# Performance work log

Measured on AMD Instinct MI355X. Metric: run time of the kernel, lower is better.

## Reference

```python
import jax, jax.numpy as jnp
import numpy as np

BS, T, D_IN = 128, 32, 128
DH = 128          # controller hidden size == memory word width M
N_SLOTS = 512     # memory rows
EPS = 1e-8


def _split_read(o):
    # o: [bs, M+6] -> k, beta, g, s(3), gamma
    k = o[:, :DH]
    beta = jax.nn.softplus(o[:, DH])
    g = jax.nn.sigmoid(o[:, DH + 1])
    s = jax.nn.softmax(o[:, DH + 2:DH + 5], axis=-1)
    gamma = 1.0 + jax.nn.softplus(o[:, DH + 5])
    return k, beta, g, s, gamma


def _attention(k, beta, g, s, gamma, mem, w_prev):
    # content addressing: cosine similarity sharpened by beta
    dot = jnp.einsum('bnm,bm->bn', mem, k)
    denom = jnp.linalg.norm(mem, axis=-1) * jnp.linalg.norm(k, axis=-1, keepdims=True) + EPS
    w_c = jax.nn.softmax(beta[:, None] * dot / denom, axis=-1)
    # gate interpolation with previous weights
    w_g = g[:, None] * w_c + (1.0 - g[:, None]) * w_prev
    # circular shift convolution over offsets {-1, 0, +1}
    w_t = (s[:, 0:1] * jnp.roll(w_g, -1, axis=-1)
           + s[:, 1:2] * w_g
           + s[:, 2:3] * jnp.roll(w_g, 1, axis=-1))
    # sharpening
    w = w_t ** gamma[:, None]
    return w / (jnp.sum(w, axis=-1, keepdims=True) + EPS)


def setup_inputs() -> dict:
    key = jax.random.key(0)
    ks = jax.random.split(key, 8)
    sc = lambda fan_in: 1.0 / np.sqrt(fan_in)
    return {
        'x':    jax.random.normal(ks[0], (BS, T, D_IN), jnp.float32),
        'Wxh':  jax.random.normal(ks[1], (D_IN, DH), jnp.float32) * sc(D_IN),
        'Whh':  jax.random.normal(ks[2], (DH, DH), jnp.float32) * sc(DH),
        'Wrh':  jax.random.normal(ks[3], (DH, DH), jnp.float32) * sc(DH),
        'bh':   jnp.zeros((DH,), jnp.float32),
        'Wout': jax.random.normal(ks[4], (DH + DH, D_IN), jnp.float32) * sc(2 * DH),
        'bout': jnp.zeros((D_IN,), jnp.float32),
        'Wr':   jax.random.normal(ks[5], (DH, DH + 6), jnp.float32) * sc(DH),
        'br':   jnp.zeros((DH + 6,), jnp.float32),
        'Ww':   jax.random.normal(ks[6], (DH, 3 * DH + 6), jnp.float32) * sc(DH),
        'bw':   jnp.zeros((3 * DH + 6,), jnp.float32),
    }


def reference(x, Wxh, Whh, Wrh, bh, Wout, bout, Wr, br, Ww, bw):
    bs = x.shape[0]
    h0 = jnp.zeros((bs, DH), x.dtype)
    r0 = jnp.zeros((bs, DH), x.dtype)
    w0 = jnp.full((bs, N_SLOTS), 1.0 / N_SLOTS, x.dtype)
    mem0 = jnp.full((bs, N_SLOTS, DH), 1e-6, x.dtype)

    def step(carry, x_t):
        h, r, w_prev, mem = carry
        # controller state
        h = jnp.tanh(x_t @ Wxh + h @ Whh + r @ Wrh + bh)
        # head parameter projections
        o_r = h @ Wr + br
        o_w = h @ Ww + bw
        k_r, b_r, g_r, s_r, y_r = _split_read(o_r)
        k_w, b_w_, g_w, s_w, y_w = _split_read(o_w[:, :DH + 6])
        e = jax.nn.sigmoid(o_w[:, DH + 6:2 * DH + 6])   # erase [bs, M]
        a = jnp.tanh(o_w[:, 2 * DH + 6:3 * DH + 6])     # add   [bs, M]
        # addressing (w_previous updated sequentially, read then write)
        w_r = _attention(k_r, b_r, g_r, s_r, y_r, mem, w_prev)
        w_w = _attention(k_w, b_w_, g_w, s_w, y_w, mem, w_r)
        # read
        r = jnp.einsum('bn,bnm->bm', w_r, mem)
        # erase / add write
        mem = mem * (1.0 - w_w[:, :, None] * e[:, None, :]) + w_w[:, :, None] * a[:, None, :]
        # output
        y = jnp.concatenate([h, r], axis=-1) @ Wout + bout
        return (h, r, w_w, mem), y

    _, ys = jax.lax.scan(step, (h0, r0, w0, mem0), jnp.swapaxes(x, 0, 1))
    return jnp.swapaxes(ys, 0, 1)  # [bs, ft, d_output]
```

## Files before the change

### kernel.cpp

```cpp
#include <hip/hip_runtime.h>
#include <hip/hip_bf16.h>
#include <math.h>

#define NT 1024
#define BSZ 128
#define TSTEPS 32
#define DIN 128
#define DHH 128
#define NSLOT 512
#define EPSF 1e-8f

static constexpr int F_FLOATS = 7160;
static constexpr size_t LDS_BYTES = 131072 + F_FLOATS * sizeof(float);

__device__ __forceinline__ float bf_lo(unsigned u) {
  union { unsigned u; float f; } c; c.u = u << 16; return c.f;
}
__device__ __forceinline__ float bf_hi(unsigned u) {
  union { unsigned u; float f; } c; c.u = u & 0xffff0000u; return c.f;
}
__device__ __forceinline__ unsigned short f2us(float f) {
  union { unsigned short s; __hip_bfloat16 h; } c; c.h = __float2bfloat16(f); return c.s;
}
__device__ __forceinline__ unsigned pkbf(float a, float b) {
  union { __hip_bfloat162 h2; unsigned u; } c;
  c.h2 = __float22bfloat162_rn(make_float2(a, b));
  return c.u;
}
__device__ __forceinline__ float sigmoid_(float x) { return 1.0f / (1.0f + __expf(-x)); }
__device__ __forceinline__ float softplus_(float x) {
  return fmaxf(x, 0.0f) + log1pf(__expf(-fabsf(x)));
}
__device__ __forceinline__ float tanh_(float x) {
  float e = __expf(-2.0f * fabsf(x));
  float t = (1.0f - e) / (1.0f + e);
  return copysignf(t, x);
}
__device__ __forceinline__ float waveSum(float v) {
#pragma unroll
  for (int m = 32; m >= 1; m >>= 1) v += __shfl_xor(v, m);
  return v;
}

__global__ __launch_bounds__(NT, 4)
void ntm_kernel(const float* __restrict__ x,
                const float* __restrict__ Wxh,
                const float* __restrict__ Whh,
                const float* __restrict__ Wrh,
                const float* __restrict__ bh,
                const float* __restrict__ Wout,
                const float* __restrict__ bout,
                const float* __restrict__ Wr,
                const float* __restrict__ br,
                const float* __restrict__ Ww,
                const float* __restrict__ bw,
                float* __restrict__ out)
{
  extern __shared__ char smem[];
  uint4* memv = (uint4*)smem;
  float* F = (float*)(smem + 131072);

  const int b = blockIdx.x;
  const int tid = threadIdx.x;
  const int g = tid >> 4, l = tid & 15;
  const int lane = tid & 63, wid = tid >> 6;

  float* U      = F + 0;
  float* yP     = F + 2560;
  float* sWprev = F + 4608;
  float* sWr    = F + 5120;
  float* sP1    = F + 5632;
  float* sOr    = F + 6144;
  float* sOw    = F + 6288;
  float* sH     = F + 6680;
  float* sR     = F + 6808;
  float* sXt    = F + 6936;
  float* sP     = F + 7064;
  uint4* krP    = (uint4*)(sP1 + 0);
  uint4* kwP    = (uint4*)(sP1 + 64);
  float* eR     = U + 0;
  float* eW     = U + 512;

  {
    const unsigned short mb = f2us(1e-6f);
    const unsigned w32 = ((unsigned)mb << 16) | mb;
    const uint4 fv = make_uint4(w32, w32, w32, w32);
    for (int i = tid; i < NSLOT * DHH / 8; i += NT) memv[i] = fv;
  }
  for (int i = tid; i < NSLOT; i += NT) sWprev[i] = 1.0f / NSLOT;
  if (tid < DHH) { sH[tid] = 0.0f; sR[tid] = 0.0f; }
  if (tid < DIN) sXt[tid] = x[(size_t)b * TSTEPS * DIN + tid];
  __syncthreads();

  for (int t = 0; t < TSTEPS; ++t) {
    {
      if (t > 0 && tid < DIN) {
        float y = bout[tid];
#pragma unroll
        for (int q = 0; q < 16; ++q) y += yP[q * 128 + tid];
        out[((size_t)b * TSTEPS + (t - 1)) * DIN + tid] = y;
      }
      const int q = tid & 63, s = tid >> 6;
      const int j2 = q * 2, i0 = s * 24;
      float2 acc = make_float2(0.f, 0.f);
#pragma unroll 8
      for (int w = 0; w < 24; ++w) {
        const int i = i0 + w;
        float v; const float* Wp;
        if (i < 128)      { v = sXt[i];       Wp = Wxh + i * DHH; }
        else if (i < 256) { v = sH[i - 128];  Wp = Whh + (i - 128) * DHH; }
        else              { v = sR[i - 256];  Wp = Wrh + (i - 256) * DHH; }
        const float2 wv = *(const float2*)(Wp + j2);
        acc.x = fmaf(v, wv.x, acc.x);
        acc.y = fmaf(v, wv.y, acc.y);
      }
      *(float2*)(U + s * 128 + j2) = acc;
      __syncthreads();
    }
    if (tid < DHH) {
      float a2 = bh[tid];
#pragma unroll
      for (int q2 = 0; q2 < 16; ++q2) a2 += U[q2 * 128 + tid];
      sH[tid] = tanh_(a2);
    }
    __syncthreads();

    {
#pragma unroll
      for (int k = 0; k < 2; ++k) {
        const int s = tid + k * NT;
        if (s < 1048) {
          const int q = (s >= 786) ? 3 : (s >= 524) ? 2 : (s >= 262) ? 1 : 0;
          const int P = s - 262 * q;
          const int i0 = 32 * q;
          const float2* p;
          int strideF2;
          if (P < 67) { p = (const float2*)(Wr + i0 * 134 + 2 * P); strideF2 = 67; }
          else        { p = (const float2*)(Ww + i0 * 390 + 2 * (P - 67)); strideF2 = 195; }
          float2 acc = make_float2(0.f, 0.f);
#pragma unroll 8
          for (int w = 0; w < 32; ++w) {
            const float v = sH[i0 + w];
            const float2 wv = *p;
            acc.x = fmaf(v, wv.x, acc.x);
            acc.y = fmaf(v, wv.y, acc.y);
            p += strideF2;
          }
          *(float2*)(U + s * 2) = acc;
        }
      }
      __syncthreads();
    }
    if (tid < 524) {
      float v = 0.f;
#pragma unroll
      for (int q = 0; q < 4; ++q) v += U[tid + 524 * q];
      if (tid < 134) sOr[tid] = v + br[tid];
      else {
        const int cw = tid - 134;
        sOw[(cw < 134) ? cw : cw + 2] = v + bw[cw];
      }
    } else if (tid >= 524 && tid < 652) {
      sR[tid - 524] = 0.f;
    } else if (tid == 1000) {
      sP[0] = 0.f; sP[1] = 0.f; sP[2] = 0.f; sP[3] = 0.f; sP[4] = 0.f; sP[5] = 0.f;
    }
    __syncthreads();
    {
      if (wid < 4) {
        float v = (tid < 128) ? sOr[tid] * sOr[tid] : sOw[tid - 128] * sOw[tid - 128];
        v = waveSum(v);
        if (lane == 0) atomicAdd(&sP[wid >> 1], v);
      } else if (tid >= 256 && tid < 384) {
        const int q = tid - 256; sOw[136 + q] = sigmoid_(sOw[136 + q]);
      } else if (tid >= 384 && tid < 512) {
        const int q = tid - 384; sOw[264 + q] = tanh_(sOw[264 + q]);
      } else if (tid >= 512 && tid < 544) {
        const int t2 = tid - 512;
        const int c = t2 & 15;
        const float* src = (t2 < 16) ? (sOr + c * 8) : (sOw + c * 8);
        union { uint4 v; unsigned short h[8]; } pk;
#pragma unroll
        for (int j = 0; j < 8; ++j) pk.h[j] = f2us(src[j]);
        if (t2 < 16) krP[c] = pk.v; else kwP[c] = pk.v;
      } else if (tid == 544) {
        sP[80] = softplus_(sOr[128]);
        sP[81] = sigmoid_(sOr[129]);
        float a0 = sOr[130], a1 = sOr[131], a2 = sOr[132];
        float mx = fmaxf(a0, fmaxf(a1, a2));
        float e0 = __expf(a0 - mx), e1 = __expf(a1 - mx), e2 = __expf(a2 - mx);
        float es = e0 + e1 + e2;
        sP[82] = e0 / es; sP[83] = e1 / es; sP[84] = e2 / es;
        sP[85] = 1.0f + softplus_(sOr[133]);
      } else if (tid == 545) {
        sP[86] = softplus_(sOw[128]);
        sP[87] = sigmoid_(sOw[129]);
        float a0 = sOw[130], a1 = sOw[131], a2 = sOw[132];
        float mx = fmaxf(a0, fmaxf(a1, a2));
        float e0 = __expf(a0 - mx), e1 = __expf(a1 - mx), e2 = __expf(a2 - mx);
        float es = e0 + e1 + e2;
        sP[88] = e0 / es; sP[89] = e1 / es; sP[90] = e2 / es;
        sP[91] = 1.0f + softplus_(sOw[133]);
      }
      __syncthreads();
    }

    {
      const float kn_r = sqrtf(sP[0]);
      const float kn_w = sqrtf(sP[1]);
      const float beta_r = sP[80], beta_w = sP[86];
      const int n = tid >> 1, hf = tid & 1;
      const int sw = (n >> 2) & 3;
      float dr = 0.f, dw = 0.f, ss = 0.f;
#pragma unroll
      for (int c = 0; c < 8; ++c) {
        const int cl = hf * 8 + c;
        const uint4 mv = memv[n * 16 + (cl ^ sw)];
        const uint4 kr = krP[cl];
        const uint4 kw = kwP[cl];
        const unsigned mw_[4] = { mv.x, mv.y, mv.z, mv.w };
        const unsigned krw[4] = { kr.x, kr.y, kr.z, kr.w };
        const unsigned kww[4] = { kw.x, kw.y, kw.z, kw.w };
#pragma unroll
        for (int j = 0; j < 4; ++j) {
          const float m0 = bf_lo(mw_[j]), m1 = bf_hi(mw_[j]);
          dr = fmaf(m0, bf_lo(krw[j]), dr); dr = fmaf(m1, bf_hi(krw[j]), dr);
          dw = fmaf(m0, bf_lo(kww[j]), dw); dw = fmaf(m1, bf_hi(kww[j]), dw);
          ss = fmaf(m0, m0, ss);            ss = fmaf(m1, m1, ss);
        }
      }
      dr += __shfl_xor(dr, 1);
      dw += __shfl_xor(dw, 1);
      ss += __shfl_xor(ss, 1);
      const float nr = sqrtf(ss);
      const float er = __expf(beta_r * dr / (nr * kn_r + EPSF));
      const float ew = __expf(beta_w * dw / (nr * kn_w + EPSF));
      if (hf == 0) { eR[n] = er; eW[n] = ew; }
      float s1 = waveSum(er) * 0.5f;
      float s2 = waveSum(ew) * 0.5f;
      if (lane == 0) { atomicAdd(&sP[2], s1); atomicAdd(&sP[3], s2); }
      __syncthreads();
    }

    {
      if (tid < NSLOT) {
        const float invE = 1.0f / sP[2];
        const float gr = sP[81], omg = 1.0f - sP[81];
        const int im = (tid - 1) & 511, ip = (tid + 1) & 511;
        const float wgm = gr * (eR[im] * invE) + omg * sWprev[im];
        const float wg0 = gr * (eR[tid] * invE) + omg * sWprev[tid];
        const float wgp = gr * (eR[ip] * invE) + omg * sWprev[ip];
        const float wt = sP[82] * wgp + sP[83] * wg0 + sP[84] * wgm;
        float p1 = (wt > 0.0f) ? __expf(sP[85] * __logf(wt)) : 0.0f;
        float P = waveSum(p1);
        sP1[tid] = p1;
        if (lane == 0) atomicAdd(&sP[4], P);
      } else {
        const int p = tid - 512;
        const int j4 = (p & 31) * 4, sl = p >> 5;
        float4 acc = make_float4(0.f, 0.f, 0.f, 0.f);
#pragma unroll
        for (int w = 0; w < 8; ++w) {
          const float v = sH[8 * sl + w];
          const float4 wv = *(const float4*)(Wout + (8 * sl + w) * DIN + j4);
          acc.x = fmaf(v, wv.x, acc.x); acc.y = fmaf(v, wv.y, acc.y);
          acc.z = fmaf(v, wv.z, acc.z); acc.w = fmaf(v, wv.w, acc.w);
        }
        *(float4*)(yP + sl * 128 + j4) = acc;
      }
      __syncthreads();
    }
    {
      if (tid < NSLOT) {
        const float pinv1 = 1.0f / (sP[4] + EPSF);
        const float invE = 1.0f / sP[3];
        const float gw = sP[87], omg = 1.0f - sP[87];
        const int im = (tid - 1) & 511, ip = (tid + 1) & 511;
        const float wgm = gw * (eW[im] * invE) + omg * (sP1[im] * pinv1);
        const float wg0 = gw * (eW[tid] * invE) + omg * (sP1[tid] * pinv1);
        const float wgp = gw * (eW[ip] * invE) + omg * (sP1[ip] * pinv1);
        sWr[tid] = sP1[tid] * pinv1;
        const float wt = sP[88] * wgp + sP[89] * wg0 + sP[90] * wgm;
        float p2 = (wt > 0.0f) ? __expf(sP[91] * __logf(wt)) : 0.0f;
        float P = waveSum(p2);
        U[tid] = p2;
        if (lane == 0) atomicAdd(&sP[5], P);
      } else if (tid < 512 + DIN && t + 1 < TSTEPS) {
        const int i = tid - 512;
        sXt[i] = x[((size_t)b * TSTEPS + (t + 1)) * DIN + i];
      }
      __syncthreads();
    }

    {
      const float pinv2 = 1.0f / (sP[5] + EPSF);
      if (tid < NSLOT) sWprev[tid] = U[tid] * pinv2;

      const int cl = l ^ ((g >> 2) & 3);
      float4 e4a = *(const float4*)(sOw + 136 + cl * 8);
      float4 e4b = *(const float4*)(sOw + 140 + cl * 8);
      float4 a4a = *(const float4*)(sOw + 264 + cl * 8);
      float4 a4b = *(const float4*)(sOw + 268 + cl * 8);
      const float e8[8] = { e4a.x, e4a.y, e4a.z, e4a.w, e4b.x, e4b.y, e4b.z, e4b.w };
      const float a8[8] = { a4a.x, a4a.y, a4a.z, a4a.w, a4b.x, a4b.y, a4b.z, a4b.w };
      float r8[8] = { 0, 0, 0, 0, 0, 0, 0, 0 };
#pragma unroll 2
      for (int it = 0; it < 8; ++it) {
        const int n = g + 64 * it;
        const float wrn = sWr[n];
        const float wwn = U[n] * pinv2;
        uint4 pk = memv[n * 16 + l];
        const unsigned wds[4] = { pk.x, pk.y, pk.z, pk.w };
        float m[8];
#pragma unroll
        for (int j = 0; j < 4; ++j) { m[2 * j] = bf_lo(wds[j]); m[2 * j + 1] = bf_hi(wds[j]); }
#pragma unroll
        for (int j = 0; j < 8; ++j) {
          r8[j] = fmaf(wrn, m[j], r8[j]);
          const float d = fmaf(-e8[j], m[j], a8[j]);
          m[j] = fmaf(wwn, d, m[j]);
        }
        pk.x = pkbf(m[0], m[1]);
        pk.y = pkbf(m[2], m[3]);
        pk.z = pkbf(m[4], m[5]);
        pk.w = pkbf(m[6], m[7]);
        memv[n * 16 + l] = pk;
      }
#pragma unroll
      for (int j = 0; j < 8; ++j) {
        r8[j] += __shfl_xor(r8[j], 16);
        r8[j] += __shfl_xor(r8[j], 32);
      }
      if (lane < 16) {
#pragma unroll
        for (int j = 0; j < 8; ++j) atomicAdd(&sR[cl * 8 + j], r8[j]);
      }
      __syncthreads();
    }

    {
      if (tid < 512) {
        const int j4 = (tid & 31) * 4, sl = tid >> 5;
        float4 acc = *(const float4*)(yP + sl * 128 + j4);
#pragma unroll
        for (int w = 0; w < 8; ++w) {
          const float v = sR[8 * sl + w];
          const float4 wv = *(const float4*)(Wout + (128 + 8 * sl + w) * DIN + j4);
          acc.x = fmaf(v, wv.x, acc.x); acc.y = fmaf(v, wv.y, acc.y);
          acc.z = fmaf(v, wv.z, acc.z); acc.w = fmaf(v, wv.w, acc.w);
        }
        *(float4*)(yP + sl * 128 + j4) = acc;
      }
      __syncthreads();
    }
  }

  if (tid < DIN) {
    float y = bout[tid];
#pragma unroll
    for (int q = 0; q < 16; ++q) y += yP[q * 128 + tid];
    out[((size_t)b * TSTEPS + (TSTEPS - 1)) * DIN + tid] = y;
  }
}

extern "C" void kernel_launch(void* const* d_in, const int* in_sizes, int n_in,
                              void* d_out, int out_size, void* d_ws, size_t ws_size,
                              hipStream_t stream) {
  (void)in_sizes; (void)n_in; (void)out_size; (void)d_ws; (void)ws_size;
  hipFuncSetAttribute(reinterpret_cast<const void*>(ntm_kernel),
                      hipFuncAttributeMaxDynamicSharedMemorySize, (int)LDS_BYTES);
  ntm_kernel<<<dim3(BSZ), dim3(NT), LDS_BYTES, stream>>>(
      (const float*)d_in[0], (const float*)d_in[1], (const float*)d_in[2],
      (const float*)d_in[3], (const float*)d_in[4], (const float*)d_in[5],
      (const float*)d_in[6], (const float*)d_in[7], (const float*)d_in[8],
      (const float*)d_in[9], (const float*)d_in[10],
      (float*)d_out);
}
```

Before: 877.3 us.

## Precompute Wxh/Whh recurrence terms in idle phases and merge projection epilogue

Splits the controller matvec so that x_t·Wxh and h·Whh are computed by otherwise idle threads during earlier phases (the sharpening phase and the output phase), leaving only r·Wrh on the critical path at each step start. It also merges the two post-projection stages (bias/reduction and activation/norm) into one phase, which removes a barrier. The bf16 packing of the key vectors is replaced by direct fp32 reads from sOr/sOw. The cost is more LDS traffic for the fp32 keys and more complex reuse of the sP1 and U regions.

```diff
diff --git a/kernel.cpp b/kernel.cpp
--- a/kernel.cpp
+++ b/kernel.cpp
@@ -76,8 +76,6 @@
   float* sR     = F + 6808;
   float* sXt    = F + 6936;
   float* sP     = F + 7064;
-  uint4* krP    = (uint4*)(sP1 + 0);
-  uint4* kwP    = (uint4*)(sP1 + 64);
   float* eR     = U + 0;
   float* eW     = U + 512;
 
@@ -90,6 +88,17 @@
   for (int i = tid; i < NSLOT; i += NT) sWprev[i] = 1.0f / NSLOT;
   if (tid < DHH) { sH[tid] = 0.0f; sR[tid] = 0.0f; }
   if (tid < DIN) sXt[tid] = x[(size_t)b * TSTEPS * DIN + tid];
+  if (tid < 512) U[2048 + tid] = 0.0f;
+  __syncthreads();
+  if (tid >= 512) {
+    const int p = tid - 512;
+    const int c = p & 127, s = p >> 7;
+    const int i0 = s * 32;
+    float acc = 0.0f;
+#pragma unroll 8
+    for (int w = 0; w < 32; ++w) acc += sXt[i0 + w] * Wxh[(i0 + w) * DHH + c];
+    sP1[s * 128 + c] = acc;
+  }
   __syncthreads();
 
   for (int t = 0; t < TSTEPS; ++t) {
@@ -101,16 +110,13 @@
         out[((size_t)b * TSTEPS + (t - 1)) * DIN + tid] = y;
       }
       const int q = tid & 63, s = tid >> 6;
-      const int j2 = q * 2, i0 = s * 24;
+      const int j2 = q * 2, i0 = s * 8;
       float2 acc = make_float2(0.f, 0.f);
-#pragma unroll 8
-      for (int w = 0; w < 24; ++w) {
+#pragma unroll
+      for (int w = 0; w < 8; ++w) {
         const int i = i0 + w;
-        float v; const float* Wp;
-        if (i < 128)      { v = sXt[i];       Wp = Wxh + i * DHH; }
-        else if (i < 256) { v = sH[i - 128];  Wp = Whh + (i - 128) * DHH; }
-        else              { v = sR[i - 256];  Wp = Wrh + (i - 256) * DHH; }
-        const float2 wv = *(const float2*)(Wp + j2);
+        const float v = sR[i];
+        const float2 wv = *(const float2*)(Wrh + i * DHH + j2);
         acc.x = fmaf(v, wv.x, acc.x);
         acc.y = fmaf(v, wv.y, acc.y);
       }
@@ -121,6 +127,10 @@
       float a2 = bh[tid];
 #pragma unroll
       for (int q2 = 0; q2 < 16; ++q2) a2 += U[q2 * 128 + tid];
+#pragma unroll
+      for (int q2 = 0; q2 < 4; ++q2) a2 += sP1[q2 * 128 + tid];
+#pragma unroll
+      for (int q2 = 0; q2 < 4; ++q2) a2 += U[2048 + q2 * 128 + tid];
       sH[tid] = tanh_(a2);
     }
     __syncthreads();
@@ -149,58 +159,73 @@
           *(float2*)(U + s * 2) = acc;
         }
       }
-      __syncthreads();
-    }
-    if (tid < 524) {
-      float v = 0.f;
-#pragma unroll
-      for (int q = 0; q < 4; ++q) v += U[tid + 524 * q];
-      if (tid < 134) sOr[tid] = v + br[tid];
-      else {
-        const int cw = tid - 134;
-        sOw[(cw < 134) ? cw : cw + 2] = v + bw[cw];
-      }
-    } else if (tid >= 524 && tid < 652) {
-      sR[tid - 524] = 0.f;
-    } else if (tid == 1000) {
-      sP[0] = 0.f; sP[1] = 0.f; sP[2] = 0.f; sP[3] = 0.f; sP[4] = 0.f; sP[5] = 0.f;
-    }
-    __syncthreads();
-    {
-      if (wid < 4) {
-        float v = (tid < 128) ? sOr[tid] * sOr[tid] : sOw[tid - 128] * sOw[tid - 128];
-        v = waveSum(v);
-        if (lane == 0) atomicAdd(&sP[wid >> 1], v);
-      } else if (tid >= 256 && tid < 384) {
-        const int q = tid - 256; sOw[136 + q] = sigmoid_(sOw[136 + q]);
-      } else if (tid >= 384 && tid < 512) {
-        const int q = tid - 384; sOw[264 + q] = tanh_(sOw[264 + q]);
-      } else if (tid >= 512 && tid < 544) {
-        const int t2 = tid - 512;
-        const int c = t2 & 15;
-        const float* src = (t2 < 16) ? (sOr + c * 8) : (sOw + c * 8);
-        union { uint4 v; unsigned short h[8]; } pk;
-#pragma unroll
-        for (int j = 0; j < 8; ++j) pk.h[j] = f2us(src[j]);
-        if (t2 < 16) krP[c] = pk.v; else kwP[c] = pk.v;
-      } else if (tid == 544) {
-        sP[80] = softplus_(sOr[128]);
-        sP[81] = sigmoid_(sOr[129]);
-        float a0 = sOr[130], a1 = sOr[131], a2 = sOr[132];
-        float mx = fmaxf(a0, fmaxf(a1, a2));
-        float e0 = __expf(a0 - mx), e1 = __expf(a1 - mx), e2 = __expf(a2 - mx);
+      if (tid == 1023) {
+        sP[0] = 0.f; sP[1] = 0.f; sP[2] = 0.f; sP[3] = 0.f; sP[4] = 0.f; sP[5] = 0.f;
+      }
+      __syncthreads();
+    }
+
+    {
+      if (tid < 134) {
+        float v = 0.f;
+#pragma unroll
+        for (int q = 0; q < 4; ++q) v += U[tid + 524 * q];
+        v += br[tid];
+        sOr[tid] = v;
+        if (tid < 128) {
+          float s2 = waveSum(v * v);
+          if (lane == 0) atomicAdd(&sP[0], s2);
+        }
+      } else if (tid == 134) {
+        float sc[6];
+#pragma unroll
+        for (int j = 0; j < 6; ++j) {
+          float v = 0.f;
+#pragma unroll
+          for (int q = 0; q < 4; ++q) v += U[(128 + j) + 524 * q];
+          sc[j] = v + br[128 + j];
+        }
+        sP[80] = softplus_(sc[0]);
+        sP[81] = sigmoid_(sc[1]);
+        float mx = fmaxf(sc[2], fmaxf(sc[3], sc[4]));
+        float e0 = __expf(sc[2] - mx), e1 = __expf(sc[3] - mx), e2 = __expf(sc[4] - mx);
         float es = e0 + e1 + e2;
         sP[82] = e0 / es; sP[83] = e1 / es; sP[84] = e2 / es;
-        sP[85] = 1.0f + softplus_(sOr[133]);
-      } else if (tid == 545) {
-        sP[86] = softplus_(sOw[128]);
-        sP[87] = sigmoid_(sOw[129]);
-        float a0 = sOw[130], a1 = sOw[131], a2 = sOw[132];
-        float mx = fmaxf(a0, fmaxf(a1, a2));
-        float e0 = __expf(a0 - mx), e1 = __expf(a1 - mx), e2 = __expf(a2 - mx);
+        sP[85] = 1.0f + softplus_(sc[5]);
+      } else if (tid == 135) {
+        float sc[6];
+#pragma unroll
+        for (int j = 0; j < 6; ++j) {
+          float v = 0.f;
+#pragma unroll
+          for (int q = 0; q < 4; ++q) v += U[(262 + j) + 524 * q];
+          sc[j] = v + bw[128 + j];
+        }
+        sP[86] = softplus_(sc[0]);
+        sP[87] = sigmoid_(sc[1]);
+        float mx = fmaxf(sc[2], fmaxf(sc[3], sc[4]));
+        float e0 = __expf(sc[2] - mx), e1 = __expf(sc[3] - mx), e2 = __expf(sc[4] - mx);
         float es = e0 + e1 + e2;
         sP[88] = e0 / es; sP[89] = e1 / es; sP[90] = e2 / es;
-        sP[91] = 1.0f + softplus_(sOw[133]);
+        sP[91] = 1.0f + softplus_(sc[5]);
+      } else if (tid >= 256 && tid < 512) {
+        const int cc = tid + 12;
+        float v = 0.f;
+#pragma unroll
+        for (int q = 0; q < 4; ++q) v += U[cc + 524 * q];
+        v += bw[tid - 122];
+        sOw[tid - 120] = (tid < 384) ? sigmoid_(v) : tanh_(v);
+      } else if (tid >= 512 && tid < 640) {
+        const int cw = tid - 512;
+        float v = 0.f;
+#pragma unroll
+        for (int q = 0; q < 4; ++q) v += U[(134 + cw) + 524 * q];
+        v += bw[cw];
+        sOw[cw] = v;
+        float s2 = waveSum(v * v);
+        if (lane == 0) atomicAdd(&sP[1], s2);
+      } else if (tid >= 640 && tid < 768) {
+        sR[tid - 640] = 0.f;
       }
       __syncthreads();
     }
@@ -216,17 +241,19 @@
       for (int c = 0; c < 8; ++c) {
         const int cl = hf * 8 + c;
         const uint4 mv = memv[n * 16 + (cl ^ sw)];
-        const uint4 kr = krP[cl];
-        const uint4 kw = kwP[cl];
+        const float4 kra = *(const float4*)(sOr + cl * 8);
+        const float4 krb = *(const float4*)(sOr + cl * 8 + 4);
+        const float4 kwa = *(const float4*)(sOw + cl * 8);
+        const float4 kwb = *(const float4*)(sOw + cl * 8 + 4);
         const unsigned mw_[4] = { mv.x, mv.y, mv.z, mv.w };
-        const unsigned krw[4] = { kr.x, kr.y, kr.z, kr.w };
-        const unsigned kww[4] = { kw.x, kw.y, kw.z, kw.w };
+        const float krf[8] = { kra.x, kra.y, kra.z, kra.w, krb.x, krb.y, krb.z, krb.w };
+        const float kwf[8] = { kwa.x, kwa.y, kwa.z, kwa.w, kwb.x, kwb.y, kwb.z, kwb.w };
 #pragma unroll
         for (int j = 0; j < 4; ++j) {
           const float m0 = bf_lo(mw_[j]), m1 = bf_hi(mw_[j]);
-          dr = fmaf(m0, bf_lo(krw[j]), dr); dr = fmaf(m1, bf_hi(krw[j]), dr);
-          dw = fmaf(m0, bf_lo(kww[j]), dw); dw = fmaf(m1, bf_hi(kww[j]), dw);
-          ss = fmaf(m0, m0, ss);            ss = fmaf(m1, m1, ss);
+          dr = fmaf(m0, krf[2 * j], dr); dr = fmaf(m1, krf[2 * j + 1], dr);
+          dw = fmaf(m0, kwf[2 * j], dw); dw = fmaf(m1, kwf[2 * j + 1], dw);
+          ss = fmaf(m0, m0, ss);         ss = fmaf(m1, m1, ss);
         }
       }
       dr += __shfl_xor(dr, 1);
@@ -285,8 +312,21 @@
         float P = waveSum(p2);
         U[tid] = p2;
         if (lane == 0) atomicAdd(&sP[5], P);
-      } else if (tid < 512 + DIN && t + 1 < TSTEPS) {
-        const int i = tid - 512;
+      } else if (tid < 768) {
+        const int p = tid - 512;
+        const int qp = p & 63, s = p >> 6;
+        const int j2 = qp * 2, i0 = s * 32;
+        float2 acc = make_float2(0.f, 0.f);
+#pragma unroll 8
+        for (int w = 0; w < 32; ++w) {
+          const float v = sH[i0 + w];
+          const float2 wv = *(const float2*)(Whh + (i0 + w) * DHH + j2);
+          acc.x = fmaf(v, wv.x, acc.x);
+          acc.y = fmaf(v, wv.y, acc.y);
+        }
+        *(float2*)(U + 2048 + s * 128 + j2) = acc;
+      } else if (tid >= 896 && t + 1 < TSTEPS) {
+        const int i = tid - 896;
         sXt[i] = x[((size_t)b * TSTEPS + (t + 1)) * DIN + i];
       }
       __syncthreads();
@@ -350,6 +390,14 @@
           acc.z = fmaf(v, wv.z, acc.z); acc.w = fmaf(v, wv.w, acc.w);
         }
         *(float4*)(yP + sl * 128 + j4) = acc;
+      } else {
+        const int p = tid - 512;
+        const int c = p & 127, s = p >> 7;
+        const int i0 = s * 32;
+        float acc = 0.0f;
+#pragma unroll 8
+        for (int w = 0; w < 32; ++w) acc += sXt[i0 + w] * Wxh[(i0 + w) * DHH + c];
+        sP1[s * 128 + c] = acc;
       }
       __syncthreads();
     }
```

New measurement: 1.167 ms. 1.33x slower.
